# Kernel tuning notes

Measured on AMD Instinct MI355X. Metric: run time of the kernel, lower is better.

The kernel has to match this reference:

```python
import jax, jax.numpy as jnp
import numpy as np

NS, NV = 64, 16
IN_DIM = NS + 3 * NV + 3 * NV + NV  # 176 = 64x0e + 16x1o + 16x1e + 16x0o
W_SHAPES = {'0e': (NS + NV, NS), '1o': (NS + 2 * NV, NV), '1e': (3 * NV, NV), '0o': (2 * NV, NV)}
W_NUMEL = sum(a * b for a, b in W_SHAPES.values())  # 7936
E = 16384
S2 = float(np.sqrt(2.0))
S3 = float(np.sqrt(3.0))


def setup_inputs() -> dict:
    key = jax.random.key(0)
    k1, k2, k3 = jax.random.split(key, 3)
    in_ = jax.random.normal(k1, (E, IN_DIM), dtype=jnp.float32)
    sh = jax.random.normal(k2, (E, 4), dtype=jnp.float32)
    weight = jax.random.normal(k3, (E, W_NUMEL), dtype=jnp.float32)
    return {"in_": in_, "sh": sh, "weight": weight}


def reference(in_, sh, weight):
    lead = in_.shape[:-1]
    # split input irreps (order: 0e, 1o, 1e, 0o)
    x0e = in_[..., :NS]                                       # [..., NS]
    x1o = in_[..., NS:NS + 3 * NV].reshape(lead + (NV, 3))    # [..., NV, 3]
    x1e = in_[..., NS + 3 * NV:NS + 6 * NV].reshape(lead + (NV, 3))
    x0o = in_[..., NS + 6 * NV:]                              # [..., NV]
    sh0 = sh[..., 0]            # [...]
    sh1 = sh[..., 1:]           # [..., 3]
    sh1b = sh1[..., None, :]    # [..., 1, 3]

    # tensor-product paths
    out0e = jnp.concatenate([
        x0e * sh0[..., None],                      # 0e x 0e -> 0e
        jnp.sum(x1o * sh1b, axis=-1) / S3,         # 1o . 1o -> 0e
    ], axis=-1)                                    # [..., NS+NV]
    out1o = jnp.concatenate([
        x0e[..., :, None] * sh1b,                  # 0e x 1o -> 1o
        x1o * sh0[..., None, None],                # 1o x 0e -> 1o
        jnp.cross(x1e, sh1b) / S2,                 # 1e x 1o -> 1o
    ], axis=-2)                                    # [..., NS+2NV, 3]
    out1e = jnp.concatenate([
        jnp.cross(x1o, sh1b) / S2,                 # 1o x 1o -> 1e
        x1e * sh0[..., None, None],                # 1e x 0e -> 1e
        x0o[..., :, None] * sh1b,                  # 0o x 1o -> 1e
    ], axis=-2)                                    # [..., 3NV, 3]
    out0o = jnp.concatenate([
        jnp.sum(x1e * sh1b, axis=-1) / S3,         # 1e . 1o -> 0o
        x0o * sh0[..., None],                      # 0o x 0e -> 0o
    ], axis=-1)                                    # [..., 2NV]

    # per-edge weights, split and path-normalized by 1/sqrt(fan_in)
    wd, off = {}, 0
    for k, (a, b) in W_SHAPES.items():
        wd[k] = weight[..., off:off + a * b].reshape(lead + (a, b)) / float(np.sqrt(a))
        off += a * b

    y0e = jnp.einsum('...i,...io->...o', out0e, wd['0e'])                     # [..., NS]
    y1o = jnp.einsum('...ic,...io->...oc', out1o, wd['1o']).reshape(lead + (3 * NV,))
    y1e = jnp.einsum('...ic,...io->...oc', out1e, wd['1e']).reshape(lead + (3 * NV,))
    y0o = jnp.einsum('...i,...io->...o', out0o, wd['0o'])                     # [..., NV]

    return jnp.concatenate([y0e, y1o, y1e, y0o], axis=-1)  # [..., 176]
```

## Files before the change

kernel.cpp:

```cpp
#include <hip/hip_runtime.h>

#define IN_DIM 176
#define W_NUMEL 7936
#define OUT_DIM 176

#define OFF_0E 0
#define OFF_1O 5120
#define OFF_1E 6656
#define OFF_0O 7424

__global__ __launch_bounds__(256)
void ftp_kernel(const float* __restrict__ in_,
                const float* __restrict__ sh,
                const float* __restrict__ weight,
                float* __restrict__ out)
{
    __shared__ float s_in[4 * 192];

    const int row = blockIdx.x;
    const int t = threadIdx.x;
    const int wave = t >> 6;
    const int l = t & 63;

    const float* __restrict__ inr = in_    + (size_t)row * IN_DIM;
    const float* __restrict__ wr  = weight + (size_t)row * W_NUMEL;
    float* __restrict__       outr= out    + (size_t)row * OUT_DIM;
    const float* __restrict__ shr = sh     + (size_t)row * 4;

    float* s_my = &s_in[wave * 192];

    const float a0 = inr[l];
    const float a1 = inr[64 + l];
    const float a2 = (l < 48) ? inr[128 + l] : 0.0f;

    const float sh0   = shr[0];
    const float sh1_0 = shr[1], sh1_1 = shr[2], sh1_2 = shr[3];

    const float inv_s3 = 0.5773502691896258f;
    const float inv_s2 = 0.7071067811865476f;

#define STAGE_AND_WAIT()                                        \
    do {                                                        \
        s_my[l] = a0; s_my[64 + l] = a1;                        \
        if (l < 48) s_my[128 + l] = a2;                         \
        __builtin_amdgcn_wave_barrier();                        \
        asm volatile("s_waitcnt lgkmcnt(0)" ::: "memory");      \
        __builtin_amdgcn_sched_barrier(0);                      \
    } while (0)

    if (wave < 2) {
        const int o4 = (wave << 3) + (l & 7);
        const int g  = l >> 3;
        float4 w[10];
        #pragma unroll
        for (int k = 0; k < 10; ++k)
            w[k] = *reinterpret_cast<const float4*>(wr + OFF_0E + (g + (k << 3)) * 64 + 4 * o4);

        STAGE_AND_WAIT();

        float s[10];
        #pragma unroll
        for (int k = 0; k < 8; ++k) s[k] = s_my[g + (k << 3)] * sh0;
        s[8] = (s_my[64 + 3*g] * sh1_0 + s_my[65 + 3*g] * sh1_1 + s_my[66 + 3*g] * sh1_2) * inv_s3;
        s[9] = (s_my[88 + 3*g] * sh1_0 + s_my[89 + 3*g] * sh1_1 + s_my[90 + 3*g] * sh1_2) * inv_s3;

        float ax = 0.f, ay = 0.f, az = 0.f, aw = 0.f;
        #pragma unroll
        for (int k = 0; k < 10; ++k) {
            ax += w[k].x * s[k]; ay += w[k].y * s[k];
            az += w[k].z * s[k]; aw += w[k].w * s[k];
        }
        #pragma unroll
        for (int m = 8; m <= 32; m <<= 1) {
            ax += __shfl_xor(ax, m); ay += __shfl_xor(ay, m);
            az += __shfl_xor(az, m); aw += __shfl_xor(aw, m);
        }
        if (g == 0) {
            const float n = 0.11180339887498949f;
            float4 r; r.x = ax*n; r.y = ay*n; r.z = az*n; r.w = aw*n;
            *reinterpret_cast<float4*>(outr + 4*o4) = r;
        }
    } else if (wave == 2) {
        const int o4 = l & 3;
        const int g  = l >> 2;
        float4 w[6];
        #pragma unroll
        for (int k = 0; k < 6; ++k)
            w[k] = *reinterpret_cast<const float4*>(wr + OFF_1O + (g + (k << 4)) * 16 + 4 * o4);

        STAGE_AND_WAIT();

        float s0[6], s1[6], s2[6];
        #pragma unroll
        for (int k = 0; k < 4; ++k) {
            const float x = s_my[g + (k << 4)];
            s0[k] = x * sh1_0; s1[k] = x * sh1_1; s2[k] = x * sh1_2;
        }
        s0[4] = s_my[64 + 3*g] * sh0;
        s1[4] = s_my[65 + 3*g] * sh0;
        s2[4] = s_my[66 + 3*g] * sh0;
        {
            const float e0 = s_my[112 + 3*g], e1 = s_my[113 + 3*g], e2 = s_my[114 + 3*g];
            s0[5] = (e1 * sh1_2 - e2 * sh1_1) * inv_s2;
            s1[5] = (e2 * sh1_0 - e0 * sh1_2) * inv_s2;
            s2[5] = (e0 * sh1_1 - e1 * sh1_0) * inv_s2;
        }

        float a0x=0,a0y=0,a0z=0,a0w=0;
        float a1x=0,a1y=0,a1z=0,a1w=0;
        float a2x=0,a2y=0,a2z=0,a2w=0;
        #pragma unroll
        for (int k = 0; k < 6; ++k) {
            a0x += w[k].x*s0[k]; a0y += w[k].y*s0[k]; a0z += w[k].z*s0[k]; a0w += w[k].w*s0[k];
            a1x += w[k].x*s1[k]; a1y += w[k].y*s1[k]; a1z += w[k].z*s1[k]; a1w += w[k].w*s1[k];
            a2x += w[k].x*s2[k]; a2y += w[k].y*s2[k]; a2z += w[k].z*s2[k]; a2w += w[k].w*s2[k];
        }
        #pragma unroll
        for (int m = 4; m <= 32; m <<= 1) {
            a0x += __shfl_xor(a0x, m); a0y += __shfl_xor(a0y, m);
            a0z += __shfl_xor(a0z, m); a0w += __shfl_xor(a0w, m);
            a1x += __shfl_xor(a1x, m); a1y += __shfl_xor(a1y, m);
            a1z += __shfl_xor(a1z, m); a1w += __shfl_xor(a1w, m);
            a2x += __shfl_xor(a2x, m); a2y += __shfl_xor(a2y, m);
            a2z += __shfl_xor(a2z, m); a2w += __shfl_xor(a2w, m);
        }
        if (g == 0) {
            const float n = 0.10206207261596575f;
            const int ob = 4*o4;
            outr[64 + (ob+0)*3 + 0] = a0x*n; outr[64 + (ob+0)*3 + 1] = a1x*n; outr[64 + (ob+0)*3 + 2] = a2x*n;
            outr[64 + (ob+1)*3 + 0] = a0y*n; outr[64 + (ob+1)*3 + 1] = a1y*n; outr[64 + (ob+1)*3 + 2] = a2y*n;
            outr[64 + (ob+2)*3 + 0] = a0z*n; outr[64 + (ob+2)*3 + 1] = a1z*n; outr[64 + (ob+2)*3 + 2] = a2z*n;
            outr[64 + (ob+3)*3 + 0] = a0w*n; outr[64 + (ob+3)*3 + 1] = a1w*n; outr[64 + (ob+3)*3 + 2] = a2w*n;
        }
    } else {
        const int o4 = l & 3;
        const int g  = l >> 2;
        float4 wa[3], wb[2];
        #pragma unroll
        for (int k = 0; k < 3; ++k)
            wa[k] = *reinterpret_cast<const float4*>(wr + OFF_1E + (g + (k << 4)) * 16 + 4 * o4);
        #pragma unroll
        for (int k = 0; k < 2; ++k)
            wb[k] = *reinterpret_cast<const float4*>(wr + OFF_0O + (g + (k << 4)) * 16 + 4 * o4);

        STAGE_AND_WAIT();

        float s0[3], s1[3], s2[3];
        {
            const float o0 = s_my[64 + 3*g], o1 = s_my[65 + 3*g], o2 = s_my[66 + 3*g];
            s0[0] = (o1 * sh1_2 - o2 * sh1_1) * inv_s2;
            s1[0] = (o2 * sh1_0 - o0 * sh1_2) * inv_s2;
            s2[0] = (o0 * sh1_1 - o1 * sh1_0) * inv_s2;
        }
        const float e0 = s_my[112 + 3*g], e1 = s_my[113 + 3*g], e2 = s_my[114 + 3*g];
        s0[1] = e0 * sh0; s1[1] = e1 * sh0; s2[1] = e2 * sh0;
        {
            const float x = s_my[160 + g];
            s0[2] = x * sh1_0; s1[2] = x * sh1_1; s2[2] = x * sh1_2;
        }

        float a0x=0,a0y=0,a0z=0,a0w=0;
        float a1x=0,a1y=0,a1z=0,a1w=0;
        float a2x=0,a2y=0,a2z=0,a2w=0;
        #pragma unroll
        for (int k = 0; k < 3; ++k) {
            a0x += wa[k].x*s0[k]; a0y += wa[k].y*s0[k]; a0z += wa[k].z*s0[k]; a0w += wa[k].w*s0[k];
            a1x += wa[k].x*s1[k]; a1y += wa[k].y*s1[k]; a1z += wa[k].z*s1[k]; a1w += wa[k].w*s1[k];
            a2x += wa[k].x*s2[k]; a2y += wa[k].y*s2[k]; a2z += wa[k].z*s2[k]; a2w += wa[k].w*s2[k];
        }
        float sb0 = (e0 * sh1_0 + e1 * sh1_1 + e2 * sh1_2) * inv_s3;
        float sb1 = s_my[160 + g] * sh0;
        float bx = wb[0].x*sb0 + wb[1].x*sb1;
        float by = wb[0].y*sb0 + wb[1].y*sb1;
        float bz = wb[0].z*sb0 + wb[1].z*sb1;
        float bw = wb[0].w*sb0 + wb[1].w*sb1;

        #pragma unroll
        for (int m = 4; m <= 32; m <<= 1) {
            a0x += __shfl_xor(a0x, m); a0y += __shfl_xor(a0y, m);
            a0z += __shfl_xor(a0z, m); a0w += __shfl_xor(a0w, m);
            a1x += __shfl_xor(a1x, m); a1y += __shfl_xor(a1y, m);
            a1z += __shfl_xor(a1z, m); a1w += __shfl_xor(a1w, m);
            a2x += __shfl_xor(a2x, m); a2y += __shfl_xor(a2y, m);
            a2z += __shfl_xor(a2z, m); a2w += __shfl_xor(a2w, m);
            bx  += __shfl_xor(bx,  m); by  += __shfl_xor(by,  m);
            bz  += __shfl_xor(bz,  m); bw  += __shfl_xor(bw,  m);
        }
        if (g == 0) {
            const float n48 = 0.14433756729740643f;
            const int ob = 4*o4;
            outr[112 + (ob+0)*3 + 0] = a0x*n48; outr[112 + (ob+0)*3 + 1] = a1x*n48; outr[112 + (ob+0)*3 + 2] = a2x*n48;
            outr[112 + (ob+1)*3 + 0] = a0y*n48; outr[112 + (ob+1)*3 + 1] = a1y*n48; outr[112 + (ob+1)*3 + 2] = a2y*n48;
            outr[112 + (ob+2)*3 + 0] = a0z*n48; outr[112 + (ob+2)*3 + 1] = a1z*n48; outr[112 + (ob+2)*3 + 2] = a2z*n48;
            outr[112 + (ob+3)*3 + 0] = a0w*n48; outr[112 + (ob+3)*3 + 1] = a1w*n48; outr[112 + (ob+3)*3 + 2] = a2w*n48;

            const float n32 = 0.17677669529663687f;
            float4 r; r.x = bx*n32; r.y = by*n32; r.z = bz*n32; r.w = bw*n32;
            *reinterpret_cast<float4*>(outr + 160 + 4*o4) = r;
        }
    }
#undef STAGE_AND_WAIT
}

extern "C" void kernel_launch(void* const* d_in, const int* in_sizes, int n_in,
                              void* d_out, int out_size, void* d_ws, size_t ws_size,
                              hipStream_t stream) {
    const float* in_    = (const float*)d_in[0];
    const float* sh     = (const float*)d_in[1];
    const float* weight = (const float*)d_in[2];
    float* out = (float*)d_out;
    const int E = in_sizes[0] / IN_DIM;

    ftp_kernel<<<E, 256, 0, stream>>>(in_, sh, weight, out);
}
```

Measured before the change: 98.29 us.

## Process two edges per block with balanced per-wave work assignment

Each 256-thread block now handles two edge rows instead of one. The per-wave tasks are rearranged so every wave does one heavy y0e half and one lighter path, balancing load that was previously skewed toward waves 0–1. The change also halves the number of blocks, raises memory-level parallelism per wave, and adds a launch_bounds occupancy hint, at the cost of more registers per thread and a tail-row guard.

```diff
diff --git a/kernel.cpp b/kernel.cpp
--- a/kernel.cpp
+++ b/kernel.cpp
@@ -9,195 +9,254 @@
 #define OFF_1E 6656
 #define OFF_0O 7424
 
-__global__ __launch_bounds__(256)
+
+__device__ __forceinline__ void load_y0e(const float* __restrict__ wr, int l, int half, float4 w[10]) {
+    const int o4 = (half << 3) + (l & 7);
+    const int g  = l >> 3;
+    #pragma unroll
+    for (int k = 0; k < 10; ++k)
+        w[k] = *reinterpret_cast<const float4*>(wr + OFF_0E + (g + (k << 3)) * 64 + 4 * o4);
+}
+
+__device__ __forceinline__ void load_y1o(const float* __restrict__ wr, int l, float4 w[6]) {
+    const int o4 = l & 3;
+    const int g  = l >> 2;
+    #pragma unroll
+    for (int k = 0; k < 6; ++k)
+        w[k] = *reinterpret_cast<const float4*>(wr + OFF_1O + (g + (k << 4)) * 16 + 4 * o4);
+}
+
+__device__ __forceinline__ void load_y1eo(const float* __restrict__ wr, int l, float4 wa[3], float4 wb[2]) {
+    const int o4 = l & 3;
+    const int g  = l >> 2;
+    #pragma unroll
+    for (int k = 0; k < 3; ++k)
+        wa[k] = *reinterpret_cast<const float4*>(wr + OFF_1E + (g + (k << 4)) * 16 + 4 * o4);
+    #pragma unroll
+    for (int k = 0; k < 2; ++k)
+        wb[k] = *reinterpret_cast<const float4*>(wr + OFF_0O + (g + (k << 4)) * 16 + 4 * o4);
+}
+
+
+__device__ __forceinline__ void comp_y0e(const float* __restrict__ s_row, const float4 w[10],
+                                         int l, int half,
+                                         float sh0, float sx, float sy, float sz,
+                                         float* __restrict__ outr, bool valid) {
+    const int o4 = (half << 3) + (l & 7);
+    const int g  = l >> 3;
+    const float inv_s3 = 0.5773502691896258f;
+    float s[10];
+    #pragma unroll
+    for (int k = 0; k < 8; ++k) s[k] = s_row[g + (k << 3)] * sh0;
+    s[8] = (s_row[64 + 3*g] * sx + s_row[65 + 3*g] * sy + s_row[66 + 3*g] * sz) * inv_s3;
+    s[9] = (s_row[88 + 3*g] * sx + s_row[89 + 3*g] * sy + s_row[90 + 3*g] * sz) * inv_s3;
+
+    float ax = 0.f, ay = 0.f, az = 0.f, aw = 0.f;
+    #pragma unroll
+    for (int k = 0; k < 10; ++k) {
+        ax += w[k].x * s[k]; ay += w[k].y * s[k];
+        az += w[k].z * s[k]; aw += w[k].w * s[k];
+    }
+    #pragma unroll
+    for (int m = 8; m <= 32; m <<= 1) {
+        ax += __shfl_xor(ax, m); ay += __shfl_xor(ay, m);
+        az += __shfl_xor(az, m); aw += __shfl_xor(aw, m);
+    }
+    if (g == 0 && valid) {
+        const float n = 0.11180339887498949f;
+        float4 r; r.x = ax*n; r.y = ay*n; r.z = az*n; r.w = aw*n;
+        *reinterpret_cast<float4*>(outr + 4*o4) = r;
+    }
+}
+
+__device__ __forceinline__ void comp_y1o(const float* __restrict__ s_row, const float4 w[6],
+                                         int l,
+                                         float sh0, float sx, float sy, float sz,
+                                         float* __restrict__ outr, bool valid) {
+    const int o4 = l & 3;
+    const int g  = l >> 2;
+    const float inv_s2 = 0.7071067811865476f;
+    float s0[6], s1[6], s2[6];
+    #pragma unroll
+    for (int k = 0; k < 4; ++k) {
+        const float x = s_row[g + (k << 4)];
+        s0[k] = x * sx; s1[k] = x * sy; s2[k] = x * sz;
+    }
+    s0[4] = s_row[64 + 3*g] * sh0;
+    s1[4] = s_row[65 + 3*g] * sh0;
+    s2[4] = s_row[66 + 3*g] * sh0;
+    {
+        const float e0 = s_row[112 + 3*g], e1 = s_row[113 + 3*g], e2 = s_row[114 + 3*g];
+        s0[5] = (e1 * sz - e2 * sy) * inv_s2;
+        s1[5] = (e2 * sx - e0 * sz) * inv_s2;
+        s2[5] = (e0 * sy - e1 * sx) * inv_s2;
+    }
+    float a0x=0,a0y=0,a0z=0,a0w=0;
+    float a1x=0,a1y=0,a1z=0,a1w=0;
+    float a2x=0,a2y=0,a2z=0,a2w=0;
+    #pragma unroll
+    for (int k = 0; k < 6; ++k) {
+        a0x += w[k].x*s0[k]; a0y += w[k].y*s0[k]; a0z += w[k].z*s0[k]; a0w += w[k].w*s0[k];
+        a1x += w[k].x*s1[k]; a1y += w[k].y*s1[k]; a1z += w[k].z*s1[k]; a1w += w[k].w*s1[k];
+        a2x += w[k].x*s2[k]; a2y += w[k].y*s2[k]; a2z += w[k].z*s2[k]; a2w += w[k].w*s2[k];
+    }
+    #pragma unroll
+    for (int m = 4; m <= 32; m <<= 1) {
+        a0x += __shfl_xor(a0x, m); a0y += __shfl_xor(a0y, m);
+        a0z += __shfl_xor(a0z, m); a0w += __shfl_xor(a0w, m);
+        a1x += __shfl_xor(a1x, m); a1y += __shfl_xor(a1y, m);
+        a1z += __shfl_xor(a1z, m); a1w += __shfl_xor(a1w, m);
+        a2x += __shfl_xor(a2x, m); a2y += __shfl_xor(a2y, m);
+        a2z += __shfl_xor(a2z, m); a2w += __shfl_xor(a2w, m);
+    }
+    if (g == 0 && valid) {
+        const float n = 0.10206207261596575f;
+        const int ob = 4*o4;
+        outr[64 + (ob+0)*3 + 0] = a0x*n; outr[64 + (ob+0)*3 + 1] = a1x*n; outr[64 + (ob+0)*3 + 2] = a2x*n;
+        outr[64 + (ob+1)*3 + 0] = a0y*n; outr[64 + (ob+1)*3 + 1] = a1y*n; outr[64 + (ob+1)*3 + 2] = a2y*n;
+        outr[64 + (ob+2)*3 + 0] = a0z*n; outr[64 + (ob+2)*3 + 1] = a1z*n; outr[64 + (ob+2)*3 + 2] = a2z*n;
+        outr[64 + (ob+3)*3 + 0] = a0w*n; outr[64 + (ob+3)*3 + 1] = a1w*n; outr[64 + (ob+3)*3 + 2] = a2w*n;
+    }
+}
+
+__device__ __forceinline__ void comp_y1eo(const float* __restrict__ s_row,
+                                          const float4 wa[3], const float4 wb[2],
+                                          int l,
+                                          float sh0, float sx, float sy, float sz,
+                                          float* __restrict__ outr, bool valid) {
+    const int o4 = l & 3;
+    const int g  = l >> 2;
+    const float inv_s2 = 0.7071067811865476f;
+    const float inv_s3 = 0.5773502691896258f;
+
+    float s0[3], s1[3], s2[3];
+    {
+        const float o0 = s_row[64 + 3*g], o1 = s_row[65 + 3*g], o2 = s_row[66 + 3*g];
+        s0[0] = (o1 * sz - o2 * sy) * inv_s2;
+        s1[0] = (o2 * sx - o0 * sz) * inv_s2;
+        s2[0] = (o0 * sy - o1 * sx) * inv_s2;
+    }
+    const float e0 = s_row[112 + 3*g], e1 = s_row[113 + 3*g], e2 = s_row[114 + 3*g];
+    s0[1] = e0 * sh0; s1[1] = e1 * sh0; s2[1] = e2 * sh0;
+    const float xo = s_row[160 + g];
+    s0[2] = xo * sx; s1[2] = xo * sy; s2[2] = xo * sz;
+
+    float a0x=0,a0y=0,a0z=0,a0w=0;
+    float a1x=0,a1y=0,a1z=0,a1w=0;
+    float a2x=0,a2y=0,a2z=0,a2w=0;
+    #pragma unroll
+    for (int k = 0; k < 3; ++k) {
+        a0x += wa[k].x*s0[k]; a0y += wa[k].y*s0[k]; a0z += wa[k].z*s0[k]; a0w += wa[k].w*s0[k];
+        a1x += wa[k].x*s1[k]; a1y += wa[k].y*s1[k]; a1z += wa[k].z*s1[k]; a1w += wa[k].w*s1[k];
+        a2x += wa[k].x*s2[k]; a2y += wa[k].y*s2[k]; a2z += wa[k].z*s2[k]; a2w += wa[k].w*s2[k];
+    }
+    float sb0 = (e0 * sx + e1 * sy + e2 * sz) * inv_s3;
+    float sb1 = xo * sh0;
+    float bx = wb[0].x*sb0 + wb[1].x*sb1;
+    float by = wb[0].y*sb0 + wb[1].y*sb1;
+    float bz = wb[0].z*sb0 + wb[1].z*sb1;
+    float bw = wb[0].w*sb0 + wb[1].w*sb1;
+
+    #pragma unroll
+    for (int m = 4; m <= 32; m <<= 1) {
+        a0x += __shfl_xor(a0x, m); a0y += __shfl_xor(a0y, m);
+        a0z += __shfl_xor(a0z, m); a0w += __shfl_xor(a0w, m);
+        a1x += __shfl_xor(a1x, m); a1y += __shfl_xor(a1y, m);
+        a1z += __shfl_xor(a1z, m); a1w += __shfl_xor(a1w, m);
+        a2x += __shfl_xor(a2x, m); a2y += __shfl_xor(a2y, m);
+        a2z += __shfl_xor(a2z, m); a2w += __shfl_xor(a2w, m);
+        bx  += __shfl_xor(bx,  m); by  += __shfl_xor(by,  m);
+        bz  += __shfl_xor(bz,  m); bw  += __shfl_xor(bw,  m);
+    }
+    if (g == 0 && valid) {
+        const float n48 = 0.14433756729740643f;
+        const int ob = 4*o4;
+        outr[112 + (ob+0)*3 + 0] = a0x*n48; outr[112 + (ob+0)*3 + 1] = a1x*n48; outr[112 + (ob+0)*3 + 2] = a2x*n48;
+        outr[112 + (ob+1)*3 + 0] = a0y*n48; outr[112 + (ob+1)*3 + 1] = a1y*n48; outr[112 + (ob+1)*3 + 2] = a2y*n48;
+        outr[112 + (ob+2)*3 + 0] = a0z*n48; outr[112 + (ob+2)*3 + 1] = a1z*n48; outr[112 + (ob+2)*3 + 2] = a2z*n48;
+        outr[112 + (ob+3)*3 + 0] = a0w*n48; outr[112 + (ob+3)*3 + 1] = a1w*n48; outr[112 + (ob+3)*3 + 2] = a2w*n48;
+
+        const float n32 = 0.17677669529663687f;
+        float4 r; r.x = bx*n32; r.y = by*n32; r.z = bz*n32; r.w = bw*n32;
+        *reinterpret_cast<float4*>(outr + 160 + 4*o4) = r;
+    }
+}
+
+
+__global__ __launch_bounds__(256, 4)
 void ftp_kernel(const float* __restrict__ in_,
                 const float* __restrict__ sh,
                 const float* __restrict__ weight,
-                float* __restrict__ out)
+                float* __restrict__ out,
+                int E)
 {
-    __shared__ float s_in[4 * 192];
-
-    const int row = blockIdx.x;
+    __shared__ float s_in[4][2][192];
+
+    const int bid = blockIdx.x;
     const int t = threadIdx.x;
     const int wave = t >> 6;
     const int l = t & 63;
 
-    const float* __restrict__ inr = in_    + (size_t)row * IN_DIM;
-    const float* __restrict__ wr  = weight + (size_t)row * W_NUMEL;
-    float* __restrict__       outr= out    + (size_t)row * OUT_DIM;
-    const float* __restrict__ shr = sh     + (size_t)row * 4;
-
-    float* s_my = &s_in[wave * 192];
-
-    const float a0 = inr[l];
-    const float a1 = inr[64 + l];
-    const float a2 = (l < 48) ? inr[128 + l] : 0.0f;
-
-    const float sh0   = shr[0];
-    const float sh1_0 = shr[1], sh1_1 = shr[2], sh1_2 = shr[3];
-
-    const float inv_s3 = 0.5773502691896258f;
-    const float inv_s2 = 0.7071067811865476f;
+    const int r0 = 2 * bid;
+    const int r1 = 2 * bid + 1;
+    const bool v1 = (r1 < E);
+    const int r1c = v1 ? r1 : r0;
+
+    const float* __restrict__ in0 = in_ + (size_t)r0 * IN_DIM;
+    const float* __restrict__ in1 = in_ + (size_t)r1c * IN_DIM;
+    const float* __restrict__ wr0 = weight + (size_t)r0 * W_NUMEL;
+    const float* __restrict__ wr1 = weight + (size_t)r1c * W_NUMEL;
+    float* __restrict__ out0 = out + (size_t)r0 * OUT_DIM;
+    float* __restrict__ out1 = out + (size_t)r1c * OUT_DIM;
+
+    const float a0 = in0[l];
+    const float a1 = in0[64 + l];
+    const float a2 = (l < 48) ? in0[128 + l] : 0.0f;
+    const float b0 = in1[l];
+    const float b1 = in1[64 + l];
+    const float b2 = (l < 48) ? in1[128 + l] : 0.0f;
+
+    const float* shr0 = sh + (size_t)r0 * 4;
+    const float* shr1 = sh + (size_t)r1c * 4;
+    const float p0 = shr0[0], px = shr0[1], py = shr0[2], pz = shr0[3];
+    const float q0 = shr1[0], qx = shr1[1], qy = shr1[2], qz = shr1[3];
+
+    float* sA = &s_in[wave][0][0];
+    float* sB = &s_in[wave][1][0];
 
 #define STAGE_AND_WAIT()                                        \
     do {                                                        \
-        s_my[l] = a0; s_my[64 + l] = a1;                        \
-        if (l < 48) s_my[128 + l] = a2;                         \
+        sA[l] = a0; sA[64 + l] = a1; if (l < 48) sA[128 + l] = a2; \
+        sB[l] = b0; sB[64 + l] = b1; if (l < 48) sB[128 + l] = b2; \
         __builtin_amdgcn_wave_barrier();                        \
         asm volatile("s_waitcnt lgkmcnt(0)" ::: "memory");      \
         __builtin_amdgcn_sched_barrier(0);                      \
     } while (0)
 
-    if (wave < 2) {
-        const int o4 = (wave << 3) + (l & 7);
-        const int g  = l >> 3;
-        float4 w[10];
-        #pragma unroll
-        for (int k = 0; k < 10; ++k)
-            w[k] = *reinterpret_cast<const float4*>(wr + OFF_0E + (g + (k << 3)) * 64 + 4 * o4);
-
-        STAGE_AND_WAIT();
-
-        float s[10];
-        #pragma unroll
-        for (int k = 0; k < 8; ++k) s[k] = s_my[g + (k << 3)] * sh0;
-        s[8] = (s_my[64 + 3*g] * sh1_0 + s_my[65 + 3*g] * sh1_1 + s_my[66 + 3*g] * sh1_2) * inv_s3;
-        s[9] = (s_my[88 + 3*g] * sh1_0 + s_my[89 + 3*g] * sh1_1 + s_my[90 + 3*g] * sh1_2) * inv_s3;
-
-        float ax = 0.f, ay = 0.f, az = 0.f, aw = 0.f;
-        #pragma unroll
-        for (int k = 0; k < 10; ++k) {
-            ax += w[k].x * s[k]; ay += w[k].y * s[k];
-            az += w[k].z * s[k]; aw += w[k].w * s[k];
-        }
-        #pragma unroll
-        for (int m = 8; m <= 32; m <<= 1) {
-            ax += __shfl_xor(ax, m); ay += __shfl_xor(ay, m);
-            az += __shfl_xor(az, m); aw += __shfl_xor(aw, m);
-        }
-        if (g == 0) {
-            const float n = 0.11180339887498949f;
-            float4 r; r.x = ax*n; r.y = ay*n; r.z = az*n; r.w = aw*n;
-            *reinterpret_cast<float4*>(outr + 4*o4) = r;
-        }
+    if (wave == 0) {
+        float4 wA[10]; load_y0e(wr0, l, 0, wA);
+        float4 wB[6];  load_y1o(wr1, l, wB);
+        STAGE_AND_WAIT();
+        comp_y0e(sA, wA, l, 0, p0, px, py, pz, out0, true);
+        comp_y1o(sB, wB, l, q0, qx, qy, qz, out1, v1);
+    } else if (wave == 1) {
+        float4 wA[10]; load_y0e(wr0, l, 1, wA);
+        float4 wa[3], wb[2]; load_y1eo(wr1, l, wa, wb);
+        STAGE_AND_WAIT();
+        comp_y0e(sA, wA, l, 1, p0, px, py, pz, out0, true);
+        comp_y1eo(sB, wa, wb, l, q0, qx, qy, qz, out1, v1);
     } else if (wave == 2) {
-        const int o4 = l & 3;
-        const int g  = l >> 2;
-        float4 w[6];
-        #pragma unroll
-        for (int k = 0; k < 6; ++k)
-            w[k] = *reinterpret_cast<const float4*>(wr + OFF_1O + (g + (k << 4)) * 16 + 4 * o4);
-
-        STAGE_AND_WAIT();
-
-        float s0[6], s1[6], s2[6];
-        #pragma unroll
-        for (int k = 0; k < 4; ++k) {
-            const float x = s_my[g + (k << 4)];
-            s0[k] = x * sh1_0; s1[k] = x * sh1_1; s2[k] = x * sh1_2;
-        }
-        s0[4] = s_my[64 + 3*g] * sh0;
-        s1[4] = s_my[65 + 3*g] * sh0;
-        s2[4] = s_my[66 + 3*g] * sh0;
-        {
-            const float e0 = s_my[112 + 3*g], e1 = s_my[113 + 3*g], e2 = s_my[114 + 3*g];
-            s0[5] = (e1 * sh1_2 - e2 * sh1_1) * inv_s2;
-            s1[5] = (e2 * sh1_0 - e0 * sh1_2) * inv_s2;
-            s2[5] = (e0 * sh1_1 - e1 * sh1_0) * inv_s2;
-        }
-
-        float a0x=0,a0y=0,a0z=0,a0w=0;
-        float a1x=0,a1y=0,a1z=0,a1w=0;
-        float a2x=0,a2y=0,a2z=0,a2w=0;
-        #pragma unroll
-        for (int k = 0; k < 6; ++k) {
-            a0x += w[k].x*s0[k]; a0y += w[k].y*s0[k]; a0z += w[k].z*s0[k]; a0w += w[k].w*s0[k];
-            a1x += w[k].x*s1[k]; a1y += w[k].y*s1[k]; a1z += w[k].z*s1[k]; a1w += w[k].w*s1[k];
-            a2x += w[k].x*s2[k]; a2y += w[k].y*s2[k]; a2z += w[k].z*s2[k]; a2w += w[k].w*s2[k];
-        }
-        #pragma unroll
-        for (int m = 4; m <= 32; m <<= 1) {
-            a0x += __shfl_xor(a0x, m); a0y += __shfl_xor(a0y, m);
-            a0z += __shfl_xor(a0z, m); a0w += __shfl_xor(a0w, m);
-            a1x += __shfl_xor(a1x, m); a1y += __shfl_xor(a1y, m);
-            a1z += __shfl_xor(a1z, m); a1w += __shfl_xor(a1w, m);
-            a2x += __shfl_xor(a2x, m); a2y += __shfl_xor(a2y, m);
-            a2z += __shfl_xor(a2z, m); a2w += __shfl_xor(a2w, m);
-        }
-        if (g == 0) {
-            const float n = 0.10206207261596575f;
-            const int ob = 4*o4;
-            outr[64 + (ob+0)*3 + 0] = a0x*n; outr[64 + (ob+0)*3 + 1] = a1x*n; outr[64 + (ob+0)*3 + 2] = a2x*n;
-            outr[64 + (ob+1)*3 + 0] = a0y*n; outr[64 + (ob+1)*3 + 1] = a1y*n; outr[64 + (ob+1)*3 + 2] = a2y*n;
-            outr[64 + (ob+2)*3 + 0] = a0z*n; outr[64 + (ob+2)*3 + 1] = a1z*n; outr[64 + (ob+2)*3 + 2] = a2z*n;
-            outr[64 + (ob+3)*3 + 0] = a0w*n; outr[64 + (ob+3)*3 + 1] = a1w*n; outr[64 + (ob+3)*3 + 2] = a2w*n;
-        }
+        float4 wA[6];  load_y1o(wr0, l, wA);
+        float4 wB[10]; load_y0e(wr1, l, 0, wB);
+        STAGE_AND_WAIT();
+        comp_y1o(sA, wA, l, p0, px, py, pz, out0, true);
+        comp_y0e(sB, wB, l, 0, q0, qx, qy, qz, out1, v1);
     } else {
-        const int o4 = l & 3;
-        const int g  = l >> 2;
-        float4 wa[3], wb[2];
-        #pragma unroll
-        for (int k = 0; k < 3; ++k)
-            wa[k] = *reinterpret_cast<const float4*>(wr + OFF_1E + (g + (k << 4)) * 16 + 4 * o4);
-        #pragma unroll
-        for (int k = 0; k < 2; ++k)
-            wb[k] = *reinterpret_cast<const float4*>(wr + OFF_0O + (g + (k << 4)) * 16 + 4 * o4);
-
-        STAGE_AND_WAIT();
-
-        float s0[3], s1[3], s2[3];
-        {
-            const float o0 = s_my[64 + 3*g], o1 = s_my[65 + 3*g], o2 = s_my[66 + 3*g];
-            s0[0] = (o1 * sh1_2 - o2 * sh1_1) * inv_s2;
-            s1[0] = (o2 * sh1_0 - o0 * sh1_2) * inv_s2;
-            s2[0] = (o0 * sh1_1 - o1 * sh1_0) * inv_s2;
-        }
-        const float e0 = s_my[112 + 3*g], e1 = s_my[113 + 3*g], e2 = s_my[114 + 3*g];
-        s0[1] = e0 * sh0; s1[1] = e1 * sh0; s2[1] = e2 * sh0;
-        {
-            const float x = s_my[160 + g];
-            s0[2] = x * sh1_0; s1[2] = x * sh1_1; s2[2] = x * sh1_2;
-        }
-
-        float a0x=0,a0y=0,a0z=0,a0w=0;
-        float a1x=0,a1y=0,a1z=0,a1w=0;
-        float a2x=0,a2y=0,a2z=0,a2w=0;
-        #pragma unroll
-        for (int k = 0; k < 3; ++k) {
-            a0x += wa[k].x*s0[k]; a0y += wa[k].y*s0[k]; a0z += wa[k].z*s0[k]; a0w += wa[k].w*s0[k];
-            a1x += wa[k].x*s1[k]; a1y += wa[k].y*s1[k]; a1z += wa[k].z*s1[k]; a1w += wa[k].w*s1[k];
-            a2x += wa[k].x*s2[k]; a2y += wa[k].y*s2[k]; a2z += wa[k].z*s2[k]; a2w += wa[k].w*s2[k];
-        }
-        float sb0 = (e0 * sh1_0 + e1 * sh1_1 + e2 * sh1_2) * inv_s3;
-        float sb1 = s_my[160 + g] * sh0;
-        float bx = wb[0].x*sb0 + wb[1].x*sb1;
-        float by = wb[0].y*sb0 + wb[1].y*sb1;
-        float bz = wb[0].z*sb0 + wb[1].z*sb1;
-        float bw = wb[0].w*sb0 + wb[1].w*sb1;
-
-        #pragma unroll
-        for (int m = 4; m <= 32; m <<= 1) {
-            a0x += __shfl_xor(a0x, m); a0y += __shfl_xor(a0y, m);
-            a0z += __shfl_xor(a0z, m); a0w += __shfl_xor(a0w, m);
-            a1x += __shfl_xor(a1x, m); a1y += __shfl_xor(a1y, m);
-            a1z += __shfl_xor(a1z, m); a1w += __shfl_xor(a1w, m);
-            a2x += __shfl_xor(a2x, m); a2y += __shfl_xor(a2y, m);
-            a2z += __shfl_xor(a2z, m); a2w += __shfl_xor(a2w, m);
-            bx  += __shfl_xor(bx,  m); by  += __shfl_xor(by,  m);
-            bz  += __shfl_xor(bz,  m); bw  += __shfl_xor(bw,  m);
-        }
-        if (g == 0) {
-            const float n48 = 0.14433756729740643f;
-            const int ob = 4*o4;
-            outr[112 + (ob+0)*3 + 0] = a0x*n48; outr[112 + (ob+0)*3 + 1] = a1x*n48; outr[112 + (ob+0)*3 + 2] = a2x*n48;
-            outr[112 + (ob+1)*3 + 0] = a0y*n48; outr[112 + (ob+1)*3 + 1] = a1y*n48; outr[112 + (ob+1)*3 + 2] = a2y*n48;
-            outr[112 + (ob+2)*3 + 0] = a0z*n48; outr[112 + (ob+2)*3 + 1] = a1z*n48; outr[112 + (ob+2)*3 + 2] = a2z*n48;
-            outr[112 + (ob+3)*3 + 0] = a0w*n48; outr[112 + (ob+3)*3 + 1] = a1w*n48; outr[112 + (ob+3)*3 + 2] = a2w*n48;
-
-            const float n32 = 0.17677669529663687f;
-            float4 r; r.x = bx*n32; r.y = by*n32; r.z = bz*n32; r.w = bw*n32;
-            *reinterpret_cast<float4*>(outr + 160 + 4*o4) = r;
-        }
+        float4 wa[3], wb[2]; load_y1eo(wr0, l, wa, wb);
+        float4 wB[10]; load_y0e(wr1, l, 1, wB);
+        STAGE_AND_WAIT();
+        comp_y1eo(sA, wa, wb, l, p0, px, py, pz, out0, true);
+        comp_y0e(sB, wB, l, 1, q0, qx, qy, qz, out1, v1);
     }
 #undef STAGE_AND_WAIT
 }
@@ -210,6 +269,7 @@
     const float* weight = (const float*)d_in[2];
     float* out = (float*)d_out;
     const int E = in_sizes[0] / IN_DIM;
-
-    ftp_kernel<<<E, 256, 0, stream>>>(in_, sh, weight, out);
-}
+    const int nblocks = (E + 1) / 2;
+
+    ftp_kernel<<<nblocks, 256, 0, stream>>>(in_, sh, weight, out, E);
+}
```

New measurement: 98.20 us. No clear change (-0.1%).
